# Performance work log

Hardware: AMD Instinct MI355X
Metric: run time of the kernel (lower is better)

The kernel has to match this reference:

```python
import jax, jax.numpy as jnp
import numpy as np

B = 131072      # batch
NC = 1000       # num_classes
A = 128         # action_dim
ELD = 128       # embedding_latent_dim
VQN = 512       # vq_num_embeddings
VQD = 64        # vq_embedding_dim
SQUISH = 1.0
CC = 0.25       # commitment cost

def _he(k, fi, fo):
    lim = float(np.sqrt(6.0 / fi))
    return jax.random.uniform(k, (fi, fo), jnp.float32, -lim, lim)

def setup_inputs() -> dict:
    key = jax.random.key(0)
    ks = jax.random.split(key, 16)
    cb_lim = float(np.sqrt(3.0 / VQD))  # variance_scaling fan_in uniform
    return {
        "obs": jax.random.randint(ks[0], (B,), 0, NC),
        "embed": jax.random.normal(ks[1], (NC, ELD), jnp.float32) * 0.02,
        "W1": _he(ks[2], ELD, 128), "b1": jnp.zeros((128,), jnp.float32),
        "W2": _he(ks[3], 128, 128), "b2": jnp.zeros((128,), jnp.float32),
        "W3": _he(ks[4], 128, 128), "b3": jnp.zeros((128,), jnp.float32),
        "Wp": _he(ks[5], 128, VQD), "bp": jnp.zeros((VQD,), jnp.float32),
        "codebook": jax.random.uniform(ks[6], (VQN, VQD), jnp.float32, -cb_lim, cb_lim),
        "Wa": jax.random.normal(ks[7], (VQD, A), jnp.float32) * 0.01, "ba": jnp.zeros((A,), jnp.float32),
        "Ws": jax.random.normal(ks[8], (VQD, A), jnp.float32) * 0.01, "bs": jnp.zeros((A,), jnp.float32),
        "Wc1": _he(ks[9], VQD, 128), "bc1": jnp.zeros((128,), jnp.float32),
        "Wc2": _he(ks[10], 128, 128), "bc2": jnp.zeros((128,), jnp.float32),
        "Wc3": _he(ks[11], 128, 32), "bc3": jnp.zeros((32,), jnp.float32),
        "Wc4": _he(ks[12], 32, 1), "bc4": jnp.zeros((1,), jnp.float32),
    }

def reference(obs, embed, W1, b1, W2, b2, W3, b3, Wp, bp, codebook,
              Wa, ba, Ws, bs, Wc1, bc1, Wc2, bc2, Wc3, bc3, Wc4, bc4):
    # embedding lookup + small dense stack
    y = jnp.take(embed, obs, axis=0)                 # [B, 128]
    z = jax.nn.relu(y @ W1 + b1)
    z = jax.nn.relu(z @ W2 + b2)
    z = jax.nn.relu(z @ W3 + b3)
    z = z @ Wp + bp                                  # [B, 64] project to vq dim
    # VQ: pairwise squared distances, argmin, gather (== one_hot @ codebook)
    d = (jnp.sum(z * z, axis=1, keepdims=True)
         - 2.0 * (z @ codebook.T)
         + jnp.sum(codebook * codebook, axis=1))     # [B, 512]
    idx = jnp.argmin(d, axis=1)                      # [B]
    quant = jnp.take(codebook, idx, axis=0)          # [B, 64]
    q = z + jax.lax.stop_gradient(quant - z)         # straight-through
    e_loss = jnp.mean((jax.lax.stop_gradient(q) - z) ** 2)
    q_loss = jnp.mean((q - jax.lax.stop_gradient(z)) ** 2)
    vq_loss = q_loss + CC * e_loss
    # actor heads (pi = MvNormalDiag(actor_mean, scale_diag); return params)
    actor_mean = jax.nn.sigmoid(q @ Wa + ba)
    scale_diag = jax.nn.sigmoid(q @ Ws + bs) * SQUISH + 1e-8
    # critic head
    c = jax.nn.sigmoid(q @ Wc1 + bc1)
    c = jax.nn.sigmoid(c @ Wc2 + bc2)
    c = jax.nn.sigmoid(c @ Wc3 + bc3)
    critic = jnp.squeeze(c @ Wc4 + bc4, axis=-1)     # [B]
    return actor_mean, scale_diag, critic, vq_loss, idx
```

## Files before the change

kernel.cpp:

```cpp
#include <hip/hip_runtime.h>
#include <math.h>


typedef float f4 __attribute__((ext_vector_type(4)));
typedef float f2 __attribute__((ext_vector_type(2)));

__device__ __forceinline__ float sigmoidf_(float x){ return 1.0f/(1.0f + expf(-x)); }

__global__ __launch_bounds__(256) void compute_kernel(
    const float* __restrict__ embed,
    const float* __restrict__ W1, const float* __restrict__ b1,
    const float* __restrict__ W2, const float* __restrict__ b2,
    const float* __restrict__ W3, const float* __restrict__ b3,
    const float* __restrict__ Wp, const float* __restrict__ bp,
    const float* __restrict__ cb,
    const float* __restrict__ Wa, const float* __restrict__ ba,
    const float* __restrict__ Ws, const float* __restrict__ bs,
    const float* __restrict__ Wc1, const float* __restrict__ bc1,
    const float* __restrict__ Wc2, const float* __restrict__ bc2,
    const float* __restrict__ Wc3, const float* __restrict__ bc3,
    const float* __restrict__ Wc4, const float* __restrict__ bc4,
    float* __restrict__ am_c, float* __restrict__ sd_c,
    float* __restrict__ cr_c, int* __restrict__ idx_t, float* __restrict__ e_t,
    float* __restrict__ loss_slot, int VQN, int NC, int nTB)
{
    const int bid = blockIdx.x;
    const int t   = threadIdx.x;
    if (bid == 0 && t == 0) *loss_slot = 0.0f;

    __shared__ double U[2][128], V[2][128];
    __shared__ double part[2][8][128];
    __shared__ double zp2[2][64];
    __shared__ float  qv2[2][64];
    __shared__ double rda[2][4];
    __shared__ int    ria[2][4];
    __shared__ int    widx2[2];
    __shared__ float  qvh[2][64];
    __shared__ float  fpart[2][4][128];
    __shared__ float  gpart[2][2][128];
    __shared__ float  h1s[2][128], h2s[2][128], h3s[2][32];

    if (bid < nTB) {
        const int c0  = bid * 2;
        const int c1  = (c0 + 1 < NC) ? c0 + 1 : NC - 1;
        const int cls = t >> 7;
        const int r   = t & 127;
        const int q4  = (t & 31) << 2;
        const int h   = t >> 5;

        if (t < 128) U[0][t] = (double)embed[(size_t)c0 * 128 + t];
        else         U[1][r] = (double)embed[(size_t)c1 * 128 + r];
        __syncthreads();

#define TRUNK2(Wm, bv, IN, OUT)                                               \
        {                                                                     \
            f4 w[16];                                                         \
            _Pragma("unroll")                                                 \
            for (int s = 0; s < 16; ++s)                                      \
                w[s] = *(const f4*)(Wm + (size_t)(h + (s << 3)) * 128 + q4);  \
            f4 bb = *(const f4*)(bv + q4);                                    \
            double aA0 = (h == 0) ? (double)bb.x : 0.0;                       \
            double aA1 = (h == 0) ? (double)bb.y : 0.0;                       \
            double aA2 = (h == 0) ? (double)bb.z : 0.0;                       \
            double aA3 = (h == 0) ? (double)bb.w : 0.0;                       \
            double aB0 = aA0, aB1 = aA1, aB2 = aA2, aB3 = aA3;                \
            _Pragma("unroll")                                                 \
            for (int s = 0; s < 16; ++s) {                                    \
                int i = h + (s << 3);                                         \
                double w0 = (double)w[s].x, w1 = (double)w[s].y;              \
                double w2 = (double)w[s].z, w3 = (double)w[s].w;              \
                double xA = IN[0][i], xB = IN[1][i];                          \
                aA0 = fma(xA, w0, aA0);  aB0 = fma(xB, w0, aB0);              \
                aA1 = fma(xA, w1, aA1);  aB1 = fma(xB, w1, aB1);              \
                aA2 = fma(xA, w2, aA2);  aB2 = fma(xB, w2, aB2);              \
                aA3 = fma(xA, w3, aA3);  aB3 = fma(xB, w3, aB3);              \
            }                                                                 \
            part[0][h][q4+0] = aA0; part[0][h][q4+1] = aA1;                   \
            part[0][h][q4+2] = aA2; part[0][h][q4+3] = aA3;                   \
            part[1][h][q4+0] = aB0; part[1][h][q4+1] = aB1;                   \
            part[1][h][q4+2] = aB2; part[1][h][q4+3] = aB3;                   \
        }                                                                     \
        __syncthreads();                                                      \
        {                                                                     \
            double acc = ((part[cls][0][r] + part[cls][1][r])                 \
                        + (part[cls][2][r] + part[cls][3][r]))                \
                       + ((part[cls][4][r] + part[cls][5][r])                 \
                        + (part[cls][6][r] + part[cls][7][r]));               \
            OUT[cls][r] = acc > 0.0 ? acc : 0.0;                              \
        }                                                                     \
        __syncthreads();

        TRUNK2(W1, b1, U, V)
        TRUNK2(W2, b2, V, U)
        TRUNK2(W3, b3, U, V)
#undef TRUNK2

        {
            const int q4p = (r & 15) << 2;
            const int hp  = r >> 4;
            f4 w[16];
            #pragma unroll
            for (int s = 0; s < 16; ++s)
                w[s] = *(const f4*)(Wp + (size_t)(hp + (s << 3)) * 64 + q4p);
            f4 bb = *(const f4*)(bp + q4p);
            double a0 = (hp == 0) ? (double)bb.x : 0.0;
            double a1 = (hp == 0) ? (double)bb.y : 0.0;
            double a2 = (hp == 0) ? (double)bb.z : 0.0;
            double a3 = (hp == 0) ? (double)bb.w : 0.0;
            #pragma unroll
            for (int s = 0; s < 16; ++s) {
                int i = hp + (s << 3);
                double x = V[cls][i];
                a0 = fma(x, (double)w[s].x, a0);
                a1 = fma(x, (double)w[s].y, a1);
                a2 = fma(x, (double)w[s].z, a2);
                a3 = fma(x, (double)w[s].w, a3);
            }
            part[cls][hp][q4p+0] = a0; part[cls][hp][q4p+1] = a1;
            part[cls][hp][q4p+2] = a2; part[cls][hp][q4p+3] = a3;
        }
        __syncthreads();
        if (r < 64) {
            zp2[cls][r] = ((part[cls][0][r] + part[cls][1][r])
                         + (part[cls][2][r] + part[cls][3][r]))
                        + ((part[cls][4][r] + part[cls][5][r])
                         + (part[cls][6][r] + part[cls][7][r]));
        }
        __syncthreads();

        double bestA = 1e300, bestB = 1e300; int biA = 0, biB = 0;
        for (int k = t; k < VQN; k += 256) {
            const float* crow = cb + (size_t)k * 64;
            f4 v[16];
            #pragma unroll
            for (int j4 = 0; j4 < 16; ++j4)
                v[j4] = *(const f4*)(crow + (j4 << 2));
            double sA0 = 0.0, sA1 = 0.0, sB0 = 0.0, sB1 = 0.0;
            #pragma unroll
            for (int j4 = 0; j4 < 16; ++j4) {
                int j = j4 << 2;
                double w0 = (double)v[j4].x, w1 = (double)v[j4].y;
                double w2 = (double)v[j4].z, w3 = (double)v[j4].w;
                double dA0 = zp2[0][j+0] - w0, dA1 = zp2[0][j+1] - w1;
                double dA2 = zp2[0][j+2] - w2, dA3 = zp2[0][j+3] - w3;
                double dB0 = zp2[1][j+0] - w0, dB1 = zp2[1][j+1] - w1;
                double dB2 = zp2[1][j+2] - w2, dB3 = zp2[1][j+3] - w3;
                sA0 = fma(dA0, dA0, sA0);  sA1 = fma(dA1, dA1, sA1);
                sA0 = fma(dA2, dA2, sA0);  sA1 = fma(dA3, dA3, sA1);
                sB0 = fma(dB0, dB0, sB0);  sB1 = fma(dB1, dB1, sB1);
                sB0 = fma(dB2, dB2, sB0);  sB1 = fma(dB3, dB3, sB1);
            }
            double sA = sA0 + sA1, sB = sB0 + sB1;
            if (sA < bestA) { bestA = sA; biA = k; }
            if (sB < bestB) { bestB = sB; biB = k; }
        }
        for (int off = 32; off > 0; off >>= 1) {
            double od = __shfl_down(bestA, off);
            int    oi = __shfl_down(biA, off);
            if (od < bestA || (od == bestA && oi < biA)) { bestA = od; biA = oi; }
            od = __shfl_down(bestB, off);
            oi = __shfl_down(biB, off);
            if (od < bestB || (od == bestB && oi < biB)) { bestB = od; biB = oi; }
        }
        {
            int wv = t >> 6;
            if ((t & 63) == 0) {
                rda[0][wv] = bestA; ria[0][wv] = biA;
                rda[1][wv] = bestB; ria[1][wv] = biB;
            }
        }
        __syncthreads();
        if (t < 2) {
            double b0 = rda[t][0]; int i0 = ria[t][0];
            for (int wv = 1; wv < 4; ++wv) {
                if (rda[t][wv] < b0 || (rda[t][wv] == b0 && ria[t][wv] < i0)) {
                    b0 = rda[t][wv]; i0 = ria[t][wv];
                }
            }
            widx2[t] = i0;
        }
        __syncthreads();
        const int widxA = widx2[0], widxB = widx2[1];
        if (t < 64)       qv2[0][t]      = cb[(size_t)widxA * 64 + t];
        else if (t < 128) qv2[1][t - 64] = cb[(size_t)widxB * 64 + (t - 64)];
        __syncthreads();

        if (t == 0) {
            idx_t[c0] = widxA;
            double e0 = 0.0, e1 = 0.0;
            for (int j = 0; j < 64; j += 2) {
                double d0 = (double)qv2[0][j]   - zp2[0][j];
                double d1 = (double)qv2[0][j+1] - zp2[0][j+1];
                e0 = fma(d0, d0, e0); e1 = fma(d1, d1, e1);
            }
            e_t[c0] = (float)(e0 + e1);
        }
        if (t == 128 && c1 != c0) {
            idx_t[c1] = widxB;
            double e0 = 0.0, e1 = 0.0;
            for (int j = 0; j < 64; j += 2) {
                double d0 = (double)qv2[1][j]   - zp2[1][j];
                double d1 = (double)qv2[1][j+1] - zp2[1][j+1];
                e0 = fma(d0, d0, e0); e1 = fma(d1, d1, e1);
            }
            e_t[c1] = (float)(e0 + e1);
        }
    } else {
        const int g  = t >> 7;
        const int tt = t & 127;
        int k = (bid - nTB) * 2 + g;
        const int kk = (k < VQN) ? k : VQN - 1;
        const int q4 = (tt & 31) << 2;

        if (tt < 64) qvh[g][tt] = cb[(size_t)kk * 64 + tt];
        __syncthreads();

        {
            const int m  = tt >> 6;
            const int hh = (tt >> 5) & 1;
            const float* Wm = m ? Ws : Wa;
            const float* bm = m ? bs : ba;
            f4 bb = *(const f4*)(bm + q4);
            float a0 = hh ? 0.0f : bb.x;
            float a1 = hh ? 0.0f : bb.y;
            float a2 = hh ? 0.0f : bb.z;
            float a3 = hh ? 0.0f : bb.w;
            f4 w[16];
            #pragma unroll
            for (int s = 0; s < 16; ++s)
                w[s] = *(const f4*)(Wm + (size_t)(hh + (s << 1)) * 128 + q4);
            #pragma unroll
            for (int s = 0; s < 16; ++s) {
                float qj = qvh[g][hh + (s << 1)];
                a0 = fmaf(qj, w[s].x, a0);
                a1 = fmaf(qj, w[s].y, a1);
                a2 = fmaf(qj, w[s].z, a2);
                a3 = fmaf(qj, w[s].w, a3);
            }
            #pragma unroll
            for (int s = 0; s < 16; ++s)
                w[s] = *(const f4*)(Wm + (size_t)(hh + ((s + 16) << 1)) * 128 + q4);
            #pragma unroll
            for (int s = 0; s < 16; ++s) {
                float qj = qvh[g][hh + ((s + 16) << 1)];
                a0 = fmaf(qj, w[s].x, a0);
                a1 = fmaf(qj, w[s].y, a1);
                a2 = fmaf(qj, w[s].z, a2);
                a3 = fmaf(qj, w[s].w, a3);
            }
            fpart[g][tt >> 5][q4+0] = a0; fpart[g][tt >> 5][q4+1] = a1;
            fpart[g][tt >> 5][q4+2] = a2; fpart[g][tt >> 5][q4+3] = a3;
        }
        __syncthreads();

        if (tt < 64) {
            const int hh = tt >> 5;
            f4 bb = *(const f4*)(bc1 + q4);
            float a0 = hh ? 0.0f : bb.x;
            float a1 = hh ? 0.0f : bb.y;
            float a2 = hh ? 0.0f : bb.z;
            float a3 = hh ? 0.0f : bb.w;
            f4 w[16];
            #pragma unroll
            for (int s = 0; s < 16; ++s)
                w[s] = *(const f4*)(Wc1 + (size_t)(hh + (s << 1)) * 128 + q4);
            #pragma unroll
            for (int s = 0; s < 16; ++s) {
                float qj = qvh[g][hh + (s << 1)];
                a0 = fmaf(qj, w[s].x, a0);
                a1 = fmaf(qj, w[s].y, a1);
                a2 = fmaf(qj, w[s].z, a2);
                a3 = fmaf(qj, w[s].w, a3);
            }
            #pragma unroll
            for (int s = 0; s < 16; ++s)
                w[s] = *(const f4*)(Wc1 + (size_t)(hh + ((s + 16) << 1)) * 128 + q4);
            #pragma unroll
            for (int s = 0; s < 16; ++s) {
                float qj = qvh[g][hh + ((s + 16) << 1)];
                a0 = fmaf(qj, w[s].x, a0);
                a1 = fmaf(qj, w[s].y, a1);
                a2 = fmaf(qj, w[s].z, a2);
                a3 = fmaf(qj, w[s].w, a3);
            }
            gpart[g][hh][q4+0] = a0; gpart[g][hh][q4+1] = a1;
            gpart[g][hh][q4+2] = a2; gpart[g][hh][q4+3] = a3;
        } else {
            int o = (tt - 64) << 1;
            am_c[(size_t)kk * 128 + o]     = sigmoidf_(fpart[g][0][o]   + fpart[g][1][o]);
            am_c[(size_t)kk * 128 + o + 1] = sigmoidf_(fpart[g][0][o+1] + fpart[g][1][o+1]);
            sd_c[(size_t)kk * 128 + o]     = sigmoidf_(fpart[g][2][o]   + fpart[g][3][o])   * 1.0f + 1e-8f;
            sd_c[(size_t)kk * 128 + o + 1] = sigmoidf_(fpart[g][2][o+1] + fpart[g][3][o+1]) * 1.0f + 1e-8f;
        }
        __syncthreads();
        h1s[g][tt] = sigmoidf_(gpart[g][0][tt] + gpart[g][1][tt]);
        __syncthreads();

        {
            const int o2 = (tt & 63) << 1;
            const int hh = tt >> 6;
            f2 bb = *(const f2*)(bc2 + o2);
            float a0 = hh ? 0.0f : bb.x;
            float a1 = hh ? 0.0f : bb.y;
            #pragma unroll
            for (int gq = 0; gq < 4; ++gq) {
                f2 w[16];
                #pragma unroll
                for (int s = 0; s < 16; ++s) {
                    int i = hh + (((gq << 4) + s) << 1);
                    w[s] = *(const f2*)(Wc2 + (size_t)i * 128 + o2);
                }
                #pragma unroll
                for (int s = 0; s < 16; ++s) {
                    int i = hh + (((gq << 4) + s) << 1);
                    float x = h1s[g][i];
                    a0 = fmaf(x, w[s].x, a0);
                    a1 = fmaf(x, w[s].y, a1);
                }
            }
            gpart[g][hh][o2+0] = a0; gpart[g][hh][o2+1] = a1;
        }
        __syncthreads();
        h2s[g][tt] = sigmoidf_(gpart[g][0][tt] + gpart[g][1][tt]);
        __syncthreads();

        if (tt < 32) {
            const int o2 = (tt & 15) << 1;
            const int hh = tt >> 4;
            f2 bb = *(const f2*)(bc3 + o2);
            float a0 = hh ? 0.0f : bb.x;
            float a1 = hh ? 0.0f : bb.y;
            #pragma unroll
            for (int gq = 0; gq < 4; ++gq) {
                f2 w[16];
                #pragma unroll
                for (int s = 0; s < 16; ++s) {
                    int i = hh + (((gq << 4) + s) << 1);
                    w[s] = *(const f2*)(Wc3 + (size_t)i * 32 + o2);
                }
                #pragma unroll
                for (int s = 0; s < 16; ++s) {
                    int i = hh + (((gq << 4) + s) << 1);
                    float x = h2s[g][i];
                    a0 = fmaf(x, w[s].x, a0);
                    a1 = fmaf(x, w[s].y, a1);
                }
            }
            gpart[g][hh][o2+0] = a0; gpart[g][hh][o2+1] = a1;
        }
        __syncthreads();
        if (tt < 32) h3s[g][tt] = sigmoidf_(gpart[g][0][tt] + gpart[g][1][tt]);
        __syncthreads();

        if (tt == 0) {
            float l4 = bc4[0];
            for (int i = 0; i < 32; ++i) l4 = fmaf(h3s[g][i], Wc4[i], l4);
            cr_c[kk] = l4;
        }
    }
}

__global__ __launch_bounds__(256) void scatter_kernel(
    const int* __restrict__ obs,
    const f4* __restrict__ am_c, const f4* __restrict__ sd_c,
    const float* __restrict__ cr_c, const int* __restrict__ idx_t,
    const float* __restrict__ e_t,
    f4* __restrict__ out_vec, float* __restrict__ out_critic,
    float* __restrict__ out_idx, float* __restrict__ out_loss,
    int B, float scale)
{
    __shared__ float red[256];
    const int vecBlocks = (B * 32) / 256;
    if ((int)blockIdx.x < vecBlocks) {
        int gid = blockIdx.x * 256 + threadIdx.x;
        int b = gid >> 5;
        int j = gid & 31;
        int k = idx_t[obs[b]];
        size_t row = (size_t)k * 32 + j;
        __builtin_nontemporal_store(am_c[row], &out_vec[gid]);
        __builtin_nontemporal_store(sd_c[row], &out_vec[(size_t)B * 32 + gid]);
        return;
    }
    int b = (blockIdx.x - vecBlocks) * 256 + threadIdx.x;
    float e = 0.0f;
    if (b < B) {
        int o = obs[b];
        int k = idx_t[o];
        __builtin_nontemporal_store(cr_c[k], &out_critic[b]);
        __builtin_nontemporal_store((float)k, &out_idx[b]);
        e = e_t[o];
    }
    red[threadIdx.x] = e;
    __syncthreads();
    for (int s = 128; s > 0; s >>= 1) {
        if (threadIdx.x < s) red[threadIdx.x] += red[threadIdx.x + s];
        __syncthreads();
    }
    if (threadIdx.x == 0) atomicAdd(out_loss, red[0] * scale);
}

extern "C" void kernel_launch(void* const* d_in, const int* in_sizes, int n_in,
                              void* d_out, int out_size, void* d_ws, size_t ws_size,
                              hipStream_t stream)
{
    const int*   obs   = (const int*)  d_in[0];
    const float* embed = (const float*)d_in[1];
    const float* W1    = (const float*)d_in[2];
    const float* b1    = (const float*)d_in[3];
    const float* W2    = (const float*)d_in[4];
    const float* b2    = (const float*)d_in[5];
    const float* W3    = (const float*)d_in[6];
    const float* b3    = (const float*)d_in[7];
    const float* Wp    = (const float*)d_in[8];
    const float* bp    = (const float*)d_in[9];
    const float* cb    = (const float*)d_in[10];
    const float* Wa    = (const float*)d_in[11];
    const float* ba    = (const float*)d_in[12];
    const float* Ws    = (const float*)d_in[13];
    const float* bs    = (const float*)d_in[14];
    const float* Wc1   = (const float*)d_in[15];
    const float* bc1   = (const float*)d_in[16];
    const float* Wc2   = (const float*)d_in[17];
    const float* bc2   = (const float*)d_in[18];
    const float* Wc3   = (const float*)d_in[19];
    const float* bc3   = (const float*)d_in[20];
    const float* Wc4   = (const float*)d_in[21];
    const float* bc4   = (const float*)d_in[22];

    const int B   = in_sizes[0];
    const int NC  = in_sizes[1] / 128;
    const int VQN = in_sizes[10] / 64;

    float* am_c = (float*)d_ws;
    float* sd_c = am_c + (size_t)VQN * 128;
    float* cr_c = sd_c + (size_t)VQN * 128;
    float* e_t  = cr_c + VQN;
    int*   idx_t = (int*)(e_t + NC);

    float* out = (float*)d_out;
    const size_t cr_off   = (size_t)B * 256;
    const size_t loss_off = cr_off + (size_t)B;
    const size_t idx_off  = loss_off + 1;

    const int nTB = (NC + 1) / 2;
    const int nHB = (VQN + 1) / 2;

    compute_kernel<<<nTB + nHB, 256, 0, stream>>>(
        embed, W1, b1, W2, b2, W3, b3, Wp, bp, cb,
        Wa, ba, Ws, bs, Wc1, bc1, Wc2, bc2, Wc3, bc3, Wc4, bc4,
        am_c, sd_c, cr_c, idx_t, e_t, out + loss_off, VQN, NC, nTB);

    const int vecBlocks    = (B * 32) / 256;
    const int scalarBlocks = (B + 255) / 256;
    scatter_kernel<<<vecBlocks + scalarBlocks, 256, 0, stream>>>(
        obs, (const f4*)am_c, (const f4*)sd_c, cr_c, idx_t, e_t,
        (f4*)out, out + cr_off, out + idx_off, out + loss_off,
        B, 1.25f / ((float)B * 64.0f));
}
```

Measured before the change: 235.2 us.

## Prefetch next-layer weights into registers ahead of compute with sched barriers

Restructures the per-class trunk and head MLPs so each layer's weights are loaded into registers one layer ahead, overlapping global loads with the previous layer's FMAs. It also issues both codebook rows at once in the VQ distance loop and loads whole head weight slices in one batch. Scheduling barriers pin the load issue order. The cost is much higher register pressure (two 16-entry f4 arrays plus up to 64-entry f2 arrays), which could reduce occupancy or cause spills.

```diff
diff --git a/kernel.cpp b/kernel.cpp
--- a/kernel.cpp
+++ b/kernel.cpp
@@ -4,6 +4,8 @@
 
 typedef float f4 __attribute__((ext_vector_type(4)));
 typedef float f2 __attribute__((ext_vector_type(2)));
+
+#define SB0() __builtin_amdgcn_sched_barrier(0)
 
 __device__ __forceinline__ float sigmoidf_(float x){ return 1.0f/(1.0f + expf(-x)); }
 
@@ -47,28 +49,21 @@
         const int r   = t & 127;
         const int q4  = (t & 31) << 2;
         const int h   = t >> 5;
-
-        if (t < 128) U[0][t] = (double)embed[(size_t)c0 * 128 + t];
-        else         U[1][r] = (double)embed[(size_t)c1 * 128 + r];
-        __syncthreads();
-
-#define TRUNK2(Wm, bv, IN, OUT)                                               \
+        const int q4p = (r & 15) << 2;
+        const int hp  = r >> 4;
+
+#define TFMA(WR, BB, IN)                                                      \
         {                                                                     \
-            f4 w[16];                                                         \
-            _Pragma("unroll")                                                 \
-            for (int s = 0; s < 16; ++s)                                      \
-                w[s] = *(const f4*)(Wm + (size_t)(h + (s << 3)) * 128 + q4);  \
-            f4 bb = *(const f4*)(bv + q4);                                    \
-            double aA0 = (h == 0) ? (double)bb.x : 0.0;                       \
-            double aA1 = (h == 0) ? (double)bb.y : 0.0;                       \
-            double aA2 = (h == 0) ? (double)bb.z : 0.0;                       \
-            double aA3 = (h == 0) ? (double)bb.w : 0.0;                       \
+            double aA0 = (h == 0) ? (double)BB.x : 0.0;                       \
+            double aA1 = (h == 0) ? (double)BB.y : 0.0;                       \
+            double aA2 = (h == 0) ? (double)BB.z : 0.0;                       \
+            double aA3 = (h == 0) ? (double)BB.w : 0.0;                       \
             double aB0 = aA0, aB1 = aA1, aB2 = aA2, aB3 = aA3;                \
             _Pragma("unroll")                                                 \
             for (int s = 0; s < 16; ++s) {                                    \
                 int i = h + (s << 3);                                         \
-                double w0 = (double)w[s].x, w1 = (double)w[s].y;              \
-                double w2 = (double)w[s].z, w3 = (double)w[s].w;              \
+                double w0 = (double)WR[s].x, w1 = (double)WR[s].y;            \
+                double w2 = (double)WR[s].z, w3 = (double)WR[s].w;            \
                 double xA = IN[0][i], xB = IN[1][i];                          \
                 aA0 = fma(xA, w0, aA0);  aB0 = fma(xB, w0, aB0);              \
                 aA1 = fma(xA, w1, aA1);  aB1 = fma(xB, w1, aB1);              \
@@ -79,7 +74,8 @@
             part[0][h][q4+2] = aA2; part[0][h][q4+3] = aA3;                   \
             part[1][h][q4+0] = aB0; part[1][h][q4+1] = aB1;                   \
             part[1][h][q4+2] = aB2; part[1][h][q4+3] = aB3;                   \
-        }                                                                     \
+        }
+#define COMBINE(OUT)                                                          \
         __syncthreads();                                                      \
         {                                                                     \
             double acc = ((part[cls][0][r] + part[cls][1][r])                 \
@@ -90,31 +86,59 @@
         }                                                                     \
         __syncthreads();
 
-        TRUNK2(W1, b1, U, V)
-        TRUNK2(W2, b2, V, U)
-        TRUNK2(W3, b3, U, V)
-#undef TRUNK2
+        f4 wa[16], wb[16];
+
+        #pragma unroll
+        for (int s = 0; s < 16; ++s)
+            wa[s] = *(const f4*)(W1 + (size_t)(h + (s << 3)) * 128 + q4);
+        f4 bb1 = *(const f4*)(b1 + q4);
+        SB0();
+        #pragma unroll
+        for (int s = 0; s < 16; ++s)
+            wb[s] = *(const f4*)(W2 + (size_t)(h + (s << 3)) * 128 + q4);
+        f4 bb2 = *(const f4*)(b2 + q4);
+        SB0();
+
+        if (t < 128) U[0][t] = (double)embed[(size_t)c0 * 128 + t];
+        else         U[1][r] = (double)embed[(size_t)c1 * 128 + r];
+        __syncthreads();
+
+        TFMA(wa, bb1, U)
+        COMBINE(V)
+
+        #pragma unroll
+        for (int s = 0; s < 16; ++s)
+            wa[s] = *(const f4*)(W3 + (size_t)(h + (s << 3)) * 128 + q4);
+        f4 bb3 = *(const f4*)(b3 + q4);
+        SB0();
+
+        TFMA(wb, bb2, V)
+        COMBINE(U)
+
+        #pragma unroll
+        for (int s = 0; s < 16; ++s)
+            wb[s] = *(const f4*)(Wp + (size_t)(hp + (s << 3)) * 64 + q4p);
+        f4 bbp = *(const f4*)(bp + q4p);
+        SB0();
+
+        TFMA(wa, bb3, U)
+        COMBINE(V)
+#undef TFMA
+#undef COMBINE
 
         {
-            const int q4p = (r & 15) << 2;
-            const int hp  = r >> 4;
-            f4 w[16];
-            #pragma unroll
-            for (int s = 0; s < 16; ++s)
-                w[s] = *(const f4*)(Wp + (size_t)(hp + (s << 3)) * 64 + q4p);
-            f4 bb = *(const f4*)(bp + q4p);
-            double a0 = (hp == 0) ? (double)bb.x : 0.0;
-            double a1 = (hp == 0) ? (double)bb.y : 0.0;
-            double a2 = (hp == 0) ? (double)bb.z : 0.0;
-            double a3 = (hp == 0) ? (double)bb.w : 0.0;
+            double a0 = (hp == 0) ? (double)bbp.x : 0.0;
+            double a1 = (hp == 0) ? (double)bbp.y : 0.0;
+            double a2 = (hp == 0) ? (double)bbp.z : 0.0;
+            double a3 = (hp == 0) ? (double)bbp.w : 0.0;
             #pragma unroll
             for (int s = 0; s < 16; ++s) {
                 int i = hp + (s << 3);
                 double x = V[cls][i];
-                a0 = fma(x, (double)w[s].x, a0);
-                a1 = fma(x, (double)w[s].y, a1);
-                a2 = fma(x, (double)w[s].z, a2);
-                a3 = fma(x, (double)w[s].w, a3);
+                a0 = fma(x, (double)wb[s].x, a0);
+                a1 = fma(x, (double)wb[s].y, a1);
+                a2 = fma(x, (double)wb[s].z, a2);
+                a3 = fma(x, (double)wb[s].w, a3);
             }
             part[cls][hp][q4p+0] = a0; part[cls][hp][q4p+1] = a1;
             part[cls][hp][q4p+2] = a2; part[cls][hp][q4p+3] = a3;
@@ -129,30 +153,64 @@
         __syncthreads();
 
         double bestA = 1e300, bestB = 1e300; int biA = 0, biB = 0;
-        for (int k = t; k < VQN; k += 256) {
-            const float* crow = cb + (size_t)k * 64;
-            f4 v[16];
-            #pragma unroll
-            for (int j4 = 0; j4 < 16; ++j4)
-                v[j4] = *(const f4*)(crow + (j4 << 2));
-            double sA0 = 0.0, sA1 = 0.0, sB0 = 0.0, sB1 = 0.0;
-            #pragma unroll
-            for (int j4 = 0; j4 < 16; ++j4) {
-                int j = j4 << 2;
-                double w0 = (double)v[j4].x, w1 = (double)v[j4].y;
-                double w2 = (double)v[j4].z, w3 = (double)v[j4].w;
-                double dA0 = zp2[0][j+0] - w0, dA1 = zp2[0][j+1] - w1;
-                double dA2 = zp2[0][j+2] - w2, dA3 = zp2[0][j+3] - w3;
-                double dB0 = zp2[1][j+0] - w0, dB1 = zp2[1][j+1] - w1;
-                double dB2 = zp2[1][j+2] - w2, dB3 = zp2[1][j+3] - w3;
-                sA0 = fma(dA0, dA0, sA0);  sA1 = fma(dA1, dA1, sA1);
-                sA0 = fma(dA2, dA2, sA0);  sA1 = fma(dA3, dA3, sA1);
-                sB0 = fma(dB0, dB0, sB0);  sB1 = fma(dB1, dB1, sB1);
-                sB0 = fma(dB2, dB2, sB0);  sB1 = fma(dB3, dB3, sB1);
-            }
-            double sA = sA0 + sA1, sB = sB0 + sB1;
-            if (sA < bestA) { bestA = sA; biA = k; }
-            if (sB < bestB) { bestB = sB; biB = k; }
+        if (VQN == 512) {
+            f4 v0[16], v1[16];
+            const float* crow0 = cb + (size_t)t * 64;
+            const float* crow1 = cb + (size_t)(t + 256) * 64;
+            #pragma unroll
+            for (int j4 = 0; j4 < 16; ++j4) v0[j4] = *(const f4*)(crow0 + (j4 << 2));
+            #pragma unroll
+            for (int j4 = 0; j4 < 16; ++j4) v1[j4] = *(const f4*)(crow1 + (j4 << 2));
+            SB0();
+            #pragma unroll
+            for (int kk2 = 0; kk2 < 2; ++kk2) {
+                double sA0 = 0.0, sA1 = 0.0, sB0 = 0.0, sB1 = 0.0;
+                #pragma unroll
+                for (int j4 = 0; j4 < 16; ++j4) {
+                    f4 v = kk2 ? v1[j4] : v0[j4];
+                    int j = j4 << 2;
+                    double w0 = (double)v.x, w1 = (double)v.y;
+                    double w2 = (double)v.z, w3 = (double)v.w;
+                    double dA0 = zp2[0][j+0] - w0, dA1 = zp2[0][j+1] - w1;
+                    double dA2 = zp2[0][j+2] - w2, dA3 = zp2[0][j+3] - w3;
+                    double dB0 = zp2[1][j+0] - w0, dB1 = zp2[1][j+1] - w1;
+                    double dB2 = zp2[1][j+2] - w2, dB3 = zp2[1][j+3] - w3;
+                    sA0 = fma(dA0, dA0, sA0);  sA1 = fma(dA1, dA1, sA1);
+                    sA0 = fma(dA2, dA2, sA0);  sA1 = fma(dA3, dA3, sA1);
+                    sB0 = fma(dB0, dB0, sB0);  sB1 = fma(dB1, dB1, sB1);
+                    sB0 = fma(dB2, dB2, sB0);  sB1 = fma(dB3, dB3, sB1);
+                }
+                double sA = sA0 + sA1, sB = sB0 + sB1;
+                int k = t + (kk2 << 8);
+                if (sA < bestA) { bestA = sA; biA = k; }
+                if (sB < bestB) { bestB = sB; biB = k; }
+            }
+        } else {
+            for (int k = t; k < VQN; k += 256) {
+                const float* crow = cb + (size_t)k * 64;
+                f4 v[16];
+                #pragma unroll
+                for (int j4 = 0; j4 < 16; ++j4) v[j4] = *(const f4*)(crow + (j4 << 2));
+                SB0();
+                double sA0 = 0.0, sA1 = 0.0, sB0 = 0.0, sB1 = 0.0;
+                #pragma unroll
+                for (int j4 = 0; j4 < 16; ++j4) {
+                    int j = j4 << 2;
+                    double w0 = (double)v[j4].x, w1 = (double)v[j4].y;
+                    double w2 = (double)v[j4].z, w3 = (double)v[j4].w;
+                    double dA0 = zp2[0][j+0] - w0, dA1 = zp2[0][j+1] - w1;
+                    double dA2 = zp2[0][j+2] - w2, dA3 = zp2[0][j+3] - w3;
+                    double dB0 = zp2[1][j+0] - w0, dB1 = zp2[1][j+1] - w1;
+                    double dB2 = zp2[1][j+2] - w2, dB3 = zp2[1][j+3] - w3;
+                    sA0 = fma(dA0, dA0, sA0);  sA1 = fma(dA1, dA1, sA1);
+                    sA0 = fma(dA2, dA2, sA0);  sA1 = fma(dA3, dA3, sA1);
+                    sB0 = fma(dB0, dB0, sB0);  sB1 = fma(dB1, dB1, sB1);
+                    sB0 = fma(dB2, dB2, sB0);  sB1 = fma(dB3, dB3, sB1);
+                }
+                double sA = sA0 + sA1, sB = sB0 + sB1;
+                if (sA < bestA) { bestA = sA; biA = k; }
+                if (sB < bestB) { bestB = sB; biB = k; }
+            }
         }
         for (int off = 32; off > 0; off >>= 1) {
             double od = __shfl_down(bestA, off);
@@ -212,76 +270,56 @@
         const int kk = (k < VQN) ? k : VQN - 1;
         const int q4 = (tt & 31) << 2;
 
+        const int m  = tt >> 6;
+        const int hh1 = (tt >> 5) & 1;
+        const float* Wm = m ? Ws : Wa;
+        const float* bm = m ? bs : ba;
+        f4 hw[32];
+        #pragma unroll
+        for (int s = 0; s < 32; ++s)
+            hw[s] = *(const f4*)(Wm + (size_t)(hh1 + (s << 1)) * 128 + q4);
+        f4 bbh = *(const f4*)(bm + q4);
+        SB0();
+
         if (tt < 64) qvh[g][tt] = cb[(size_t)kk * 64 + tt];
         __syncthreads();
 
         {
-            const int m  = tt >> 6;
-            const int hh = (tt >> 5) & 1;
-            const float* Wm = m ? Ws : Wa;
-            const float* bm = m ? bs : ba;
-            f4 bb = *(const f4*)(bm + q4);
+            float a0 = hh1 ? 0.0f : bbh.x;
+            float a1 = hh1 ? 0.0f : bbh.y;
+            float a2 = hh1 ? 0.0f : bbh.z;
+            float a3 = hh1 ? 0.0f : bbh.w;
+            #pragma unroll
+            for (int s = 0; s < 32; ++s) {
+                float qj = qvh[g][hh1 + (s << 1)];
+                a0 = fmaf(qj, hw[s].x, a0);
+                a1 = fmaf(qj, hw[s].y, a1);
+                a2 = fmaf(qj, hw[s].z, a2);
+                a3 = fmaf(qj, hw[s].w, a3);
+            }
+            fpart[g][tt >> 5][q4+0] = a0; fpart[g][tt >> 5][q4+1] = a1;
+            fpart[g][tt >> 5][q4+2] = a2; fpart[g][tt >> 5][q4+3] = a3;
+        }
+        __syncthreads();
+
+        if (tt < 64) {
+            const int hh = tt >> 5;
+            #pragma unroll
+            for (int s = 0; s < 32; ++s)
+                hw[s] = *(const f4*)(Wc1 + (size_t)(hh + (s << 1)) * 128 + q4);
+            f4 bb = *(const f4*)(bc1 + q4);
+            SB0();
             float a0 = hh ? 0.0f : bb.x;
             float a1 = hh ? 0.0f : bb.y;
             float a2 = hh ? 0.0f : bb.z;
             float a3 = hh ? 0.0f : bb.w;
-            f4 w[16];
-            #pragma unroll
-            for (int s = 0; s < 16; ++s)
-                w[s] = *(const f4*)(Wm + (size_t)(hh + (s << 1)) * 128 + q4);
-            #pragma unroll
-            for (int s = 0; s < 16; ++s) {
+            #pragma unroll
+            for (int s = 0; s < 32; ++s) {
                 float qj = qvh[g][hh + (s << 1)];
-                a0 = fmaf(qj, w[s].x, a0);
-                a1 = fmaf(qj, w[s].y, a1);
-                a2 = fmaf(qj, w[s].z, a2);
-                a3 = fmaf(qj, w[s].w, a3);
-            }
-            #pragma unroll
-            for (int s = 0; s < 16; ++s)
-                w[s] = *(const f4*)(Wm + (size_t)(hh + ((s + 16) << 1)) * 128 + q4);
-            #pragma unroll
-            for (int s = 0; s < 16; ++s) {
-                float qj = qvh[g][hh + ((s + 16) << 1)];
-                a0 = fmaf(qj, w[s].x, a0);
-                a1 = fmaf(qj, w[s].y, a1);
-                a2 = fmaf(qj, w[s].z, a2);
-                a3 = fmaf(qj, w[s].w, a3);
-            }
-            fpart[g][tt >> 5][q4+0] = a0; fpart[g][tt >> 5][q4+1] = a1;
-            fpart[g][tt >> 5][q4+2] = a2; fpart[g][tt >> 5][q4+3] = a3;
-        }
-        __syncthreads();
-
-        if (tt < 64) {
-            const int hh = tt >> 5;
-            f4 bb = *(const f4*)(bc1 + q4);
-            float a0 = hh ? 0.0f : bb.x;
-            float a1 = hh ? 0.0f : bb.y;
-            float a2 = hh ? 0.0f : bb.z;
-            float a3 = hh ? 0.0f : bb.w;
-            f4 w[16];
-            #pragma unroll
-            for (int s = 0; s < 16; ++s)
-                w[s] = *(const f4*)(Wc1 + (size_t)(hh + (s << 1)) * 128 + q4);
-            #pragma unroll
-            for (int s = 0; s < 16; ++s) {
-                float qj = qvh[g][hh + (s << 1)];
-                a0 = fmaf(qj, w[s].x, a0);
-                a1 = fmaf(qj, w[s].y, a1);
-                a2 = fmaf(qj, w[s].z, a2);
-                a3 = fmaf(qj, w[s].w, a3);
-            }
-            #pragma unroll
-            for (int s = 0; s < 16; ++s)
-                w[s] = *(const f4*)(Wc1 + (size_t)(hh + ((s + 16) << 1)) * 128 + q4);
-            #pragma unroll
-            for (int s = 0; s < 16; ++s) {
-                float qj = qvh[g][hh + ((s + 16) << 1)];
-                a0 = fmaf(qj, w[s].x, a0);
-                a1 = fmaf(qj, w[s].y, a1);
-                a2 = fmaf(qj, w[s].z, a2);
-                a3 = fmaf(qj, w[s].w, a3);
+                a0 = fmaf(qj, hw[s].x, a0);
+                a1 = fmaf(qj, hw[s].y, a1);
+                a2 = fmaf(qj, hw[s].z, a2);
+                a3 = fmaf(qj, hw[s].w, a3);
             }
             gpart[g][hh][q4+0] = a0; gpart[g][hh][q4+1] = a1;
             gpart[g][hh][q4+2] = a2; gpart[g][hh][q4+3] = a3;
@@ -299,24 +337,19 @@
         {
             const int o2 = (tt & 63) << 1;
             const int hh = tt >> 6;
+            f2 cw[64];
+            #pragma unroll
+            for (int s = 0; s < 64; ++s)
+                cw[s] = *(const f2*)(Wc2 + (size_t)(hh + (s << 1)) * 128 + o2);
             f2 bb = *(const f2*)(bc2 + o2);
+            SB0();
             float a0 = hh ? 0.0f : bb.x;
             float a1 = hh ? 0.0f : bb.y;
             #pragma unroll
-            for (int gq = 0; gq < 4; ++gq) {
-                f2 w[16];
-                #pragma unroll
-                for (int s = 0; s < 16; ++s) {
-                    int i = hh + (((gq << 4) + s) << 1);
-                    w[s] = *(const f2*)(Wc2 + (size_t)i * 128 + o2);
-                }
-                #pragma unroll
-                for (int s = 0; s < 16; ++s) {
-                    int i = hh + (((gq << 4) + s) << 1);
-                    float x = h1s[g][i];
-                    a0 = fmaf(x, w[s].x, a0);
-                    a1 = fmaf(x, w[s].y, a1);
-                }
+            for (int s = 0; s < 64; ++s) {
+                float x = h1s[g][hh + (s << 1)];
+                a0 = fmaf(x, cw[s].x, a0);
+                a1 = fmaf(x, cw[s].y, a1);
             }
             gpart[g][hh][o2+0] = a0; gpart[g][hh][o2+1] = a1;
         }
@@ -327,24 +360,19 @@
         if (tt < 32) {
             const int o2 = (tt & 15) << 1;
             const int hh = tt >> 4;
+            f2 cw[64];
+            #pragma unroll
+            for (int s = 0; s < 64; ++s)
+                cw[s] = *(const f2*)(Wc3 + (size_t)(hh + (s << 1)) * 32 + o2);
             f2 bb = *(const f2*)(bc3 + o2);
+            SB0();
             float a0 = hh ? 0.0f : bb.x;
             float a1 = hh ? 0.0f : bb.y;
             #pragma unroll
-            for (int gq = 0; gq < 4; ++gq) {
-                f2 w[16];
-                #pragma unroll
-                for (int s = 0; s < 16; ++s) {
-                    int i = hh + (((gq << 4) + s) << 1);
-                    w[s] = *(const f2*)(Wc3 + (size_t)i * 32 + o2);
-                }
-                #pragma unroll
-                for (int s = 0; s < 16; ++s) {
-                    int i = hh + (((gq << 4) + s) << 1);
-                    float x = h2s[g][i];
-                    a0 = fmaf(x, w[s].x, a0);
-                    a1 = fmaf(x, w[s].y, a1);
-                }
+            for (int s = 0; s < 64; ++s) {
+                float x = h2s[g][hh + (s << 1)];
+                a0 = fmaf(x, cw[s].x, a0);
+                a1 = fmaf(x, cw[s].y, a1);
             }
             gpart[g][hh][o2+0] = a0; gpart[g][hh][o2+1] = a1;
         }
@@ -353,8 +381,18 @@
         __syncthreads();
 
         if (tt == 0) {
+            f4 w4[8];
+            #pragma unroll
+            for (int s = 0; s < 8; ++s) w4[s] = *(const f4*)(Wc4 + (s << 2));
+            SB0();
             float l4 = bc4[0];
-            for (int i = 0; i < 32; ++i) l4 = fmaf(h3s[g][i], Wc4[i], l4);
+            #pragma unroll
+            for (int i = 0; i < 32; ++i) {
+                float wv = (i & 3) == 0 ? w4[i >> 2].x :
+                           (i & 3) == 1 ? w4[i >> 2].y :
+                           (i & 3) == 2 ? w4[i >> 2].z : w4[i >> 2].w;
+                l4 = fmaf(h3s[g][i], wv, l4);
+            }
             cr_c[kk] = l4;
         }
     }
```

After: 237.6 us. About the same (+1.0%).
